# Performance work log

Hardware: AMD Instinct MI355X
Metric: run time of the kernel (lower is better)

Reference implementation:

```python
import jax, jax.numpy as jnp
import numpy as np

B, D, N, H, K = 4, 1024, 4096, 16, 128
DH = D // H  # per-head dim (note: torch view splits D as (DH, H) in that order)
BN_EPS = 1e-3


def conv1(x, w, b):
    # 1x1 Conv1d == channel matmul: x [B,Cin,N], w [Cout,Cin], b [Cout]
    return jnp.einsum('oi,bin->bon', w, x) + b[None, :, None]


def setup_inputs() -> dict:
    key = jax.random.key(0)
    ks = jax.random.split(key, 16)
    s = 0.02
    proj_std = 1.0 / np.sqrt(K)  # init_() uniform(-1/sqrt(k), 1/sqrt(k))
    return {
        'x': jax.random.normal(ks[0], (B, D, N), jnp.float32),
        'source': jax.random.normal(ks[1], (B, D, N), jnp.float32),
        'to_q_w': jax.random.normal(ks[2], (D, D), jnp.float32) * s,
        'to_q_b': jnp.zeros((D,), jnp.float32),
        'to_k_w': jax.random.normal(ks[3], (D, D), jnp.float32) * s,
        'to_k_b': jnp.zeros((D,), jnp.float32),
        'proj_k': jax.random.uniform(ks[4], (N, K), jnp.float32, -proj_std, proj_std),
        'merge_w': jax.random.normal(ks[5], (D, D), jnp.float32) * s,
        'merge_b': jnp.zeros((D,), jnp.float32),
        'mlp_w1': jax.random.normal(ks[6], (2 * D, 2 * D), jnp.float32) * s,
        'mlp_b1': jnp.zeros((2 * D,), jnp.float32),
        'bn_gamma': jnp.ones((2 * D,), jnp.float32),
        'bn_beta': jnp.zeros((2 * D,), jnp.float32),
        'bn_mean': jnp.zeros((2 * D,), jnp.float32),
        'bn_var': jnp.ones((2 * D,), jnp.float32),
        'mlp_w2': jax.random.normal(ks[7], (D, 2 * D), jnp.float32) * s,
        'mlp_b2': jnp.zeros((D,), jnp.float32),
    }


def reference(x, source, to_q_w, to_q_b, to_k_w, to_k_b, proj_k, merge_w, merge_b,
              mlp_w1, mlp_b1, bn_gamma, bn_beta, bn_mean, bn_var, mlp_w2, mlp_b2):
    b = x.shape[0]
    q = conv1(x, to_q_w, to_q_b)          # [B,D,N]
    k = conv1(source, to_k_w, to_k_b)     # [B,D,M]
    v = k                                  # share_kv=True
    # Linformer sequence-length reduction: M -> K (proj_v == proj_k when shared)
    k = jnp.einsum('bdm,mk->bdk', k, proj_k)   # [B,D,K]
    v = jnp.einsum('bdm,mk->bdk', v, proj_k)   # [B,D,K]
    # torch .view(B, dim, heads, -1): channel axis split as (DH, H)
    qh = q.reshape(b, DH, H, N)
    kh = k.reshape(b, DH, H, K)
    vh = v.reshape(b, DH, H, K)
    scores = jnp.einsum('bdhn,bdhk->bhnk', qh, kh) / (DH ** 0.5)
    prob = jax.nn.softmax(scores, axis=-1)      # [B,H,N,K], small K
    msg = jnp.einsum('bhnk,bdhk->bdhn', prob, vh).reshape(b, D, N)
    msg = conv1(msg, merge_w, merge_b)
    # MLP([2D, 2D, D]): conv -> BN(eval, eps=1e-3) -> ReLU -> conv
    h = jnp.concatenate([x, msg], axis=1)       # [B,2D,N]
    h = conv1(h, mlp_w1, mlp_b1)
    h = bn_gamma[None, :, None] * (h - bn_mean[None, :, None]) \
        * jax.lax.rsqrt(bn_var + BN_EPS)[None, :, None] + bn_beta[None, :, None]
    h = jax.nn.relu(h)
    return conv1(h, mlp_w2, mlp_b2)             # [B,D,N]
```

## Files before the change

### kernel.cpp

```cpp
#include <hip/hip_runtime.h>
#include <stdint.h>

typedef __bf16 bf16x8 __attribute__((ext_vector_type(8)));
typedef float f32x4 __attribute__((ext_vector_type(4)));

__device__ __forceinline__ unsigned short f2bf(float f) {
    union { float f; uint32_t i; } v;
    v.f = f;
    uint32_t x = v.i;
    return (unsigned short)((x + 0x7FFFu + ((x >> 16) & 1u)) >> 16);
}

typedef __attribute__((address_space(3))) unsigned int lds_u32;
typedef __attribute__((address_space(1))) const unsigned int glob_u32;
__device__ __forceinline__ void gld16(const unsigned short* g, unsigned short* l) {
    __builtin_amdgcn_global_load_lds((glob_u32*)g, (lds_u32*)l, 16, 0, 0);
}

__global__ __launch_bounds__(256) void prep_weights(
    const float* __restrict__ Wq, const float* __restrict__ Wk,
    const float* __restrict__ Wm, const float* __restrict__ W1,
    const float* __restrict__ W2, const float* __restrict__ bq,
    const float* __restrict__ bk,
    unsigned short* __restrict__ wqb, unsigned short* __restrict__ wkb,
    unsigned short* __restrict__ wmb, unsigned short* __restrict__ w1b,
    unsigned short* __restrict__ w2b, float* __restrict__ bqp,
    float* __restrict__ bkp)
{
    const int b = blockIdx.x, t = threadIdx.x;
    if (b < 2048) {
        const float* in = (b < 1024) ? Wq : Wk;
        unsigned short* out = (b < 1024) ? wqb : wkb;
        const int i = ((b & 1023) * 256 + t) * 4;
        const int row = i >> 10, col = i & 1023;
        const float4 v = *(const float4*)(in + ((row & 63) * 16 + (row >> 6)) * 1024 + col);
        out[i + 0] = f2bf(v.x); out[i + 1] = f2bf(v.y);
        out[i + 2] = f2bf(v.z); out[i + 3] = f2bf(v.w);
    } else if (b < 3072) {
        const int i = ((b - 2048) * 256 + t) * 4;
        const int row = i >> 10, c0 = i & 1023;
        const float* r = Wm + (size_t)row * 1024;
#pragma unroll
        for (int j = 0; j < 4; ++j) {
            const int c = c0 + j;
            wmb[i + j] = f2bf(r[(c & 63) * 16 + (c >> 6)]);
        }
    } else if (b < 7168) {
        const int i = ((b - 3072) * 256 + t) * 4;
        const float4 v = *(const float4*)(W1 + i);
        w1b[i + 0] = f2bf(v.x); w1b[i + 1] = f2bf(v.y);
        w1b[i + 2] = f2bf(v.z); w1b[i + 3] = f2bf(v.w);
    } else if (b < 9216) {
        const int i = ((b - 7168) * 256 + t) * 4;
        const float4 v = *(const float4*)(W2 + i);
        w2b[i + 0] = f2bf(v.x); w2b[i + 1] = f2bf(v.y);
        w2b[i + 2] = f2bf(v.z); w2b[i + 3] = f2bf(v.w);
    } else {
        const int o = (b - 9216) * 256 + t;
        const int src = (o & 63) * 16 + (o >> 6);
        bqp[o] = bq[src];
        bkp[o] = bk[src];
    }
}

__global__ __launch_bounds__(256) void cvt_transpose(
    const float* __restrict__ in, unsigned short* __restrict__ out,
    int R, int C)
{
    __shared__ unsigned short tile[32][33];
    const size_t bo = (size_t)blockIdx.z * R * C;
    const int c0 = blockIdx.x * 32, r0 = blockIdx.y * 32;
    const int tx = threadIdx.x & 31, ty = threadIdx.x >> 5;
#pragma unroll
    for (int i = 0; i < 4; ++i)
        tile[ty + i * 8][tx] = f2bf(in[bo + (size_t)(r0 + ty + i * 8) * C + (c0 + tx)]);
    __syncthreads();
#pragma unroll
    for (int i = 0; i < 4; ++i)
        out[bo + (size_t)(c0 + ty + i * 8) * R + (r0 + tx)] = tile[tx][ty + i * 8];
}

__global__ __launch_bounds__(256) void cvt_transpose_xs(
    const float* __restrict__ x, const float* __restrict__ s,
    unsigned short* __restrict__ xt, unsigned short* __restrict__ st)
{
    __shared__ unsigned short tile[32][33];
    const int z = blockIdx.z;
    const float* in = (z < 4) ? x : s;
    unsigned short* out = (z < 4) ? xt : st;
    const size_t bo = (size_t)(z & 3) * 1024 * 4096;
    const int c0 = blockIdx.x * 32, r0 = blockIdx.y * 32;
    const int tx = threadIdx.x & 31, ty = threadIdx.x >> 5;
#pragma unroll
    for (int i = 0; i < 4; ++i)
        tile[ty + i * 8][tx] = f2bf(in[bo + (size_t)(r0 + ty + i * 8) * 4096 + (c0 + tx)]);
    __syncthreads();
#pragma unroll
    for (int i = 0; i < 4; ++i)
        out[bo + (size_t)(c0 + ty + i * 8) * 1024 + (r0 + tx)] = tile[tx][ty + i * 8];
}

template<int LDA, int LDB, int LDC, int KD, int SPLIT, bool CONCAT>
__global__ __launch_bounds__(256) void gemm_bt(
    const unsigned short* __restrict__ A,
    const unsigned short* __restrict__ A2, int K1,
    const unsigned short* __restrict__ BT,
    unsigned short* __restrict__ C, float* __restrict__ Cf,
    long long strideA, long long strideB, long long strideC,
    const float* __restrict__ bias_m,
    const float* __restrict__ bias_n,
    const float* __restrict__ bn_g,
    const float* __restrict__ bn_b,
    const float* __restrict__ bn_mu,
    const float* __restrict__ bn_var)
{
    constexpr int KPB = KD / SPLIT;
    __shared__ __align__(16) unsigned short As[128 * 64];
    __shared__ __align__(16) unsigned short Bs[128 * 64];

    const int z = blockIdx.z;
    const int batch = z / SPLIT;
    const int kbase = (z % SPLIT) * KPB;
    const int m0 = blockIdx.y * 128, n0 = blockIdx.x * 128;
    const unsigned short* Ab  = A + (size_t)batch * strideA;
    const unsigned short* A2b = CONCAT ? A2 + (size_t)batch * strideA
                                       : (const unsigned short*)0;
    const unsigned short* Bb = BT + (size_t)batch * strideB;

    const int t = threadIdx.x;
    const int lane = t & 63, wid = t >> 6;
    const int wm = wid >> 1, wn = wid & 1;
    const int r16 = lane & 15, quad = lane >> 4;

    f32x4 acc[4][4];
    const f32x4 zf = {0.f, 0.f, 0.f, 0.f};
#pragma unroll
    for (int i = 0; i < 4; ++i)
#pragma unroll
        for (int j = 0; j < 4; ++j) acc[i][j] = zf;

    for (int kt = kbase; kt < kbase + KPB; kt += 64) {
        const unsigned short* Asrc = Ab;
        int kk = kt;
        if (CONCAT && kt >= K1) { Asrc = A2b; kk = kt - K1; }
#pragma unroll
        for (int i = 0; i < 4; ++i) {
            const int p = i * 256 + t;
            const int row = p >> 3, slot = p & 7;
            const int kc = (slot ^ (row & 7)) * 8;
            gld16(&Asrc[(size_t)(m0 + row) * LDA + kk + kc], &As[p * 8]);
            gld16(&Bb[(size_t)(n0 + row) * LDB + kt + kc], &Bs[p * 8]);
        }
        __syncthreads();
#pragma unroll
        for (int s = 0; s < 2; ++s) {
            bf16x8 af[4], bfb[4];
#pragma unroll
            for (int i = 0; i < 4; ++i) {
                const int ra = wm * 64 + i * 16 + r16;
                const int rb = wn * 64 + i * 16 + r16;
                af[i]  = *(const bf16x8*)&As[(ra * 8 + ((s * 4 + quad) ^ (ra & 7))) * 8];
                bfb[i] = *(const bf16x8*)&Bs[(rb * 8 + ((s * 4 + quad) ^ (rb & 7))) * 8];
            }
#pragma unroll
            for (int mi = 0; mi < 4; ++mi)
#pragma unroll
                for (int ni = 0; ni < 4; ++ni)
                    acc[mi][ni] = __builtin_amdgcn_mfma_f32_16x16x32_bf16(
                        af[mi], bfb[ni], acc[mi][ni], 0, 0, 0);
        }
        __syncthreads();
    }

    unsigned short* Cb = C ? C + (size_t)z * strideC : (unsigned short*)0;
    float* Cfb = Cf ? Cf + (size_t)z * strideC : (float*)0;
    const bool has_bn = (bn_g != 0);
#pragma unroll
    for (int ni = 0; ni < 4; ++ni) {
        const int gn = n0 + wn * 64 + ni * 16 + r16;
        const float addn = bias_n ? bias_n[gn] : 0.f;
        float g = 1.f, bb = 0.f, mu = 0.f, rstd = 1.f;
        if (has_bn) {
            g = bn_g[gn]; bb = bn_b[gn]; mu = bn_mu[gn];
            rstd = rsqrtf(bn_var[gn] + 1e-3f);
        }
#pragma unroll
        for (int mi = 0; mi < 4; ++mi) {
            const int gm0 = m0 + wm * 64 + mi * 16 + quad * 4;
#pragma unroll
            for (int r = 0; r < 4; ++r) {
                float v = acc[mi][ni][r] + addn;
                if (bias_m) v += bias_m[gm0 + r];
                if (has_bn) { v = g * (v - mu) * rstd + bb; v = fmaxf(v, 0.f); }
                const size_t idx = (size_t)(gm0 + r) * LDC + gn;
                if (Cfb) Cfb[idx] = v;
                else     Cb[idx]  = f2bf(v);
            }
        }
    }
}

__global__ __launch_bounds__(256) void reduce_kp(
    const float* __restrict__ acc, unsigned short* __restrict__ kpb)
{
    const int j = (blockIdx.x * 256 + threadIdx.x) * 4;
    const int b = j >> 17, jj = j & 131071;
    const float* base = acc + (size_t)b * 8 * 131072 + jj;
    float4 s = *(const float4*)base;
#pragma unroll
    for (int p = 1; p < 8; ++p) {
        const float4 v = *(const float4*)(base + (size_t)p * 131072);
        s.x += v.x; s.y += v.y; s.z += v.z; s.w += v.w;
    }
    kpb[j + 0] = f2bf(s.x); kpb[j + 1] = f2bf(s.y);
    kpb[j + 2] = f2bf(s.z); kpb[j + 3] = f2bf(s.w);
}

__global__ __launch_bounds__(256) void attn_fused(
    const unsigned short* __restrict__ qT,
    const unsigned short* __restrict__ kp,
    unsigned short* __restrict__ msgT)
{
    constexpr int QS = 72, KS = 72, VS = 136, PS = 136;
    __shared__ __align__(16) unsigned short QKP[128 * QS + 128 * KS];
    __shared__ __align__(16) unsigned short Vs[64 * VS];
    unsigned short* Qs = QKP;
    unsigned short* Ks = QKP + 128 * QS;
    unsigned short* Ps = QKP;

    const int t = threadIdx.x;
    const int lane = t & 63, w = t >> 6;
    const int r16 = lane & 15, quad = lane >> 4;
    const int h = blockIdx.y, n0 = blockIdx.x * 128;
    const size_t b = blockIdx.z;

    const unsigned short* qbase = qT + (b * 4096 + n0) * 1024 + h * 64;
    const unsigned short* kbase = kp + (b * 1024 + h * 64) * 128;

#pragma unroll
    for (int i = 0; i < 4; ++i) {
        const int c = i * 256 + t;
        const int n = c >> 3, dh0 = (c & 7) * 8;
        *(int4*)&Qs[n * QS + dh0] = *(const int4*)&qbase[(size_t)n * 1024 + dh0];
    }
#pragma unroll
    for (int i = 0; i < 4; ++i) {
        const int c = i * 256 + t;
        const int kkq = c & 3, dh = (c >> 2) & 63, kkh = c >> 8;
        const int kk0 = kkh * 32 + kkq * 8;
        const bf16x8 v = *(const bf16x8*)&kbase[(size_t)dh * 128 + kk0];
        *(bf16x8*)&Vs[dh * VS + kk0] = v;
        const unsigned short* vs = (const unsigned short*)&v;
#pragma unroll
        for (int j = 0; j < 8; ++j) Ks[(kk0 + j) * KS + dh] = vs[j];
    }
    __syncthreads();

    f32x4 S[2][8];
    const f32x4 zf = {0.f, 0.f, 0.f, 0.f};
#pragma unroll
    for (int mi = 0; mi < 2; ++mi)
#pragma unroll
        for (int ni = 0; ni < 8; ++ni) S[mi][ni] = zf;

    bf16x8 aq[2][2];
#pragma unroll
    for (int mi = 0; mi < 2; ++mi)
#pragma unroll
        for (int ks = 0; ks < 2; ++ks)
            aq[mi][ks] = *(const bf16x8*)&Qs[(w * 32 + mi * 16 + r16) * QS + ks * 32 + quad * 8];
#pragma unroll
    for (int ni = 0; ni < 8; ++ni) {
        const bf16x8 b0 = *(const bf16x8*)&Ks[(ni * 16 + r16) * KS + quad * 8];
        const bf16x8 b1 = *(const bf16x8*)&Ks[(ni * 16 + r16) * KS + 32 + quad * 8];
#pragma unroll
        for (int mi = 0; mi < 2; ++mi) {
            S[mi][ni] = __builtin_amdgcn_mfma_f32_16x16x32_bf16(aq[mi][0], b0, S[mi][ni], 0, 0, 0);
            S[mi][ni] = __builtin_amdgcn_mfma_f32_16x16x32_bf16(aq[mi][1], b1, S[mi][ni], 0, 0, 0);
        }
    }

    __syncthreads();

    float linv[2][4];
#pragma unroll
    for (int mi = 0; mi < 2; ++mi) {
        float e[8][4];
        float rs0 = 0.f, rs1 = 0.f, rs2 = 0.f, rs3 = 0.f;
#pragma unroll
        for (int ni = 0; ni < 8; ++ni) {
            e[ni][0] = __expf(S[mi][ni][0] * 0.125f); rs0 += e[ni][0];
            e[ni][1] = __expf(S[mi][ni][1] * 0.125f); rs1 += e[ni][1];
            e[ni][2] = __expf(S[mi][ni][2] * 0.125f); rs2 += e[ni][2];
            e[ni][3] = __expf(S[mi][ni][3] * 0.125f); rs3 += e[ni][3];
        }
        float rs[4] = {rs0, rs1, rs2, rs3};
#pragma unroll
        for (int r = 0; r < 4; ++r) {
            float s = rs[r];
            s += __shfl_xor(s, 1); s += __shfl_xor(s, 2);
            s += __shfl_xor(s, 4); s += __shfl_xor(s, 8);
            linv[mi][r] = 1.f / s;
        }
#pragma unroll
        for (int ni = 0; ni < 8; ++ni)
#pragma unroll
            for (int r = 0; r < 4; ++r)
                Ps[(w * 32 + mi * 16 + quad * 4 + r) * PS + ni * 16 + r16] = f2bf(e[ni][r]);
    }
    __syncthreads();

    f32x4 O[2][4];
#pragma unroll
    for (int mi = 0; mi < 2; ++mi)
#pragma unroll
        for (int ni = 0; ni < 4; ++ni) O[mi][ni] = zf;

    bf16x8 ap[2][4];
#pragma unroll
    for (int mi = 0; mi < 2; ++mi)
#pragma unroll
        for (int ks = 0; ks < 4; ++ks)
            ap[mi][ks] = *(const bf16x8*)&Ps[(w * 32 + mi * 16 + r16) * PS + ks * 32 + quad * 8];
#pragma unroll
    for (int ni = 0; ni < 4; ++ni)
#pragma unroll
        for (int ks = 0; ks < 4; ++ks) {
            const bf16x8 bv = *(const bf16x8*)&Vs[(ni * 16 + r16) * VS + ks * 32 + quad * 8];
#pragma unroll
            for (int mi = 0; mi < 2; ++mi)
                O[mi][ni] = __builtin_amdgcn_mfma_f32_16x16x32_bf16(ap[mi][ks], bv, O[mi][ni], 0, 0, 0);
        }

    unsigned short* ob = msgT + (b * 4096 + n0) * 1024 + h * 64;
#pragma unroll
    for (int mi = 0; mi < 2; ++mi)
#pragma unroll
        for (int ni = 0; ni < 4; ++ni)
#pragma unroll
            for (int r = 0; r < 4; ++r)
                ob[(size_t)(w * 32 + mi * 16 + quad * 4 + r) * 1024 + ni * 16 + r16] =
                    f2bf(O[mi][ni][r] * linv[mi][r]);
}

extern "C" void kernel_launch(void* const* d_in, const int* in_sizes, int n_in,
                              void* d_out, int out_size, void* d_ws, size_t ws_size,
                              hipStream_t stream)
{
    (void)in_sizes; (void)n_in; (void)out_size; (void)ws_size;
    const float* x    = (const float*)d_in[0];
    const float* srcp = (const float*)d_in[1];
    const float* Wq   = (const float*)d_in[2];
    const float* bq   = (const float*)d_in[3];
    const float* Wk   = (const float*)d_in[4];
    const float* bk   = (const float*)d_in[5];
    const float* proj = (const float*)d_in[6];
    const float* Wm   = (const float*)d_in[7];
    const float* bm   = (const float*)d_in[8];
    const float* W1   = (const float*)d_in[9];
    const float* b1   = (const float*)d_in[10];
    const float* gam  = (const float*)d_in[11];
    const float* bet  = (const float*)d_in[12];
    const float* mu   = (const float*)d_in[13];
    const float* var  = (const float*)d_in[14];
    const float* W2   = (const float*)d_in[15];
    const float* b2   = (const float*)d_in[16];
    float* out = (float*)d_out;
    unsigned short* ws = (unsigned short*)d_ws;

    const long long E = 16777216LL;
    unsigned short* xt  = ws;
    unsigned short* st  = xt + E;
    unsigned short* qt  = st + E;
    unsigned short* kc  = qt + E;
    unsigned short* ht  = kc + E;
    unsigned short* pT  = ht + 2 * E;
    unsigned short* kpb = pT + 524288;
    unsigned short* wqb = kpb + 524288;
    unsigned short* wkb = wqb + 1048576;
    unsigned short* wmb = wkb + 1048576;
    unsigned short* w1b = wmb + 1048576;
    unsigned short* w2b = w1b + 4194304;
    float* bqp = (float*)(w2b + 2097152);
    float* bkp = bqp + 1024;
    float* kpacc = (float*)ht;

    cvt_transpose_xs<<<dim3(128, 32, 8), 256, 0, stream>>>(x, srcp, xt, st);
    cvt_transpose<<<dim3(4, 128, 1), 256, 0, stream>>>(proj, pT, 4096, 128);
    prep_weights<<<9220, 256, 0, stream>>>(Wq, Wk, Wm, W1, W2, bq, bk,
                                           wqb, wkb, wmb, w1b, w2b, bqp, bkp);

    gemm_bt<1024, 1024, 1024, 1024, 1, false><<<dim3(8, 32, 4), 256, 0, stream>>>(
        xt, nullptr, 1024, wqb, qt, nullptr,
        4096LL * 1024, 0LL, 4096LL * 1024, nullptr, bqp,
        nullptr, nullptr, nullptr, nullptr);
    gemm_bt<1024, 1024, 4096, 1024, 1, false><<<dim3(32, 8, 4), 256, 0, stream>>>(
        wkb, nullptr, 1024, st, kc, nullptr,
        0LL, 4096LL * 1024, 1024LL * 4096, bkp, nullptr,
        nullptr, nullptr, nullptr, nullptr);
    gemm_bt<4096, 4096, 128, 4096, 8, false><<<dim3(1, 8, 32), 256, 0, stream>>>(
        kc, nullptr, 4096, pT, nullptr, kpacc,
        1024LL * 4096, 0LL, 1024LL * 128, nullptr, nullptr,
        nullptr, nullptr, nullptr, nullptr);
    reduce_kp<<<512, 256, 0, stream>>>(kpacc, kpb);
    attn_fused<<<dim3(32, 16, 4), 256, 0, stream>>>(qt, kpb, qt);
    gemm_bt<1024, 1024, 1024, 1024, 1, false><<<dim3(8, 32, 4), 256, 0, stream>>>(
        qt, nullptr, 1024, wmb, st, nullptr,
        4096LL * 1024, 0LL, 4096LL * 1024, nullptr, bm,
        nullptr, nullptr, nullptr, nullptr);
    gemm_bt<1024, 2048, 2048, 2048, 1, true><<<dim3(16, 32, 4), 256, 0, stream>>>(
        xt, st, 1024, w1b, ht, nullptr,
        4096LL * 1024, 0LL, 4096LL * 2048, nullptr, b1,
        gam, bet, mu, var);
    gemm_bt<2048, 2048, 4096, 2048, 1, false><<<dim3(32, 8, 4), 256, 0, stream>>>(
        w2b, nullptr, 2048, ht, nullptr, out,
        0LL, 4096LL * 2048, 1024LL * 4096, b2, nullptr,
        nullptr, nullptr, nullptr, nullptr);
}
```

Before: 727.0 us.

## Add 256x256 double-buffered 8-wave GEMM kernel for projection and MLP GEMMs

Introduces a new gemm256 kernel with 256x256 output tiles, 512 threads, double-buffered LDS filled by direct global-to-LDS loads, XOR-swizzled layout, interleaved load/MFMA phases with setprio, and an XCD-aware block remap. It replaces the previous gemm_bt launches for the Q, K, merge, and both MLP GEMMs. The aim is higher arithmetic intensity and better overlap of memory loads with MFMA work. It also uses much more LDS (128KB per block), which may limit occupancy, and the grids are smaller, which could leave CUs underused.

After: 667.8 us. -8.1%, faster.

```diff
diff --git a/kernel.cpp b/kernel.cpp
--- a/kernel.cpp
+++ b/kernel.cpp
@@ -199,6 +199,183 @@
         }
     }
 }
+
+#define BAR   __builtin_amdgcn_s_barrier()
+#define LGKM0 asm volatile("s_waitcnt lgkmcnt(0)" ::: "memory")
+#define PRIO1 __builtin_amdgcn_s_setprio(1)
+#define PRIO0 __builtin_amdgcn_s_setprio(0)
+
+#define ST_A(dst, kt, i0, i1) do {                                          \
+    const unsigned short* S_ = Ab; long long kk_ = (kt);                    \
+    if (CONCAT && (kt) >= K1) { S_ = A2b; kk_ = (kt) - K1; }                \
+    gld16(&S_[offA[i0] + kk_], (dst) + po[i0]);                             \
+    gld16(&S_[offA[i1] + kk_], (dst) + po[i1]); } while (0)
+
+#define ST_B(dst, kt, i0, i1) do {                                          \
+    gld16(&Bb[offB[i0] + (kt)], (dst) + po[i0]);                            \
+    gld16(&Bb[offB[i1] + (kt)], (dst) + po[i1]); } while (0)
+
+#define RD_A(mh, AC) do {                                                   \
+    _Pragma("unroll") for (int mi = 0; mi < 4; ++mi) {                      \
+        const int ra = wm * 128 + (mh) * 64 + mi * 16 + r16;                \
+        _Pragma("unroll") for (int ks = 0; ks < 2; ++ks) {                  \
+            const int c_ = ks * 4 + quad;                                   \
+            a[mi][ks] = *(const bf16x8*)&(AC)[(ra * 8 + (c_ ^ (ra & 7))) * 8]; \
+        } } } while (0)
+
+#define RD_B(np, BC) do {                                                   \
+    _Pragma("unroll") for (int i = 0; i < 2; ++i) {                         \
+        const int rb = wn * 64 + ((np) * 2 + i) * 16 + r16;                 \
+        _Pragma("unroll") for (int ks = 0; ks < 2; ++ks) {                  \
+            const int c_ = ks * 4 + quad;                                   \
+            b[(np) * 2 + i][ks] = *(const bf16x8*)&(BC)[(rb * 8 + (c_ ^ (rb & 7))) * 8]; \
+        } } } while (0)
+
+#define MFMA_PH(mh, np) do {                                                \
+    _Pragma("unroll") for (int mi = 0; mi < 4; ++mi)                        \
+    _Pragma("unroll") for (int i = 0; i < 2; ++i)                           \
+    _Pragma("unroll") for (int ks = 0; ks < 2; ++ks)                        \
+        acc[(mh) * 4 + mi][(np) * 2 + i] =                                  \
+            __builtin_amdgcn_mfma_f32_16x16x32_bf16(                        \
+                a[mi][ks], b[(np) * 2 + i][ks],                             \
+                acc[(mh) * 4 + mi][(np) * 2 + i], 0, 0, 0); } while (0)
+
+#define TILE_BODY(XV, AC, BC, AN, BN_) do {                                 \
+    const int kt1_ = ((XV) + 1) * 64, kt2_ = ((XV) + 2) * 64;               \
+    const bool g1_ = ((XV) + 1) < nt, g2_ = ((XV) + 2) < nt;                \
+         \
+    RD_A(0, AC); RD_B(0, BC);                                               \
+    if (g1_) ST_A(AN, kt1_, 1, 3);                                          \
+    BAR; LGKM0; PRIO1; MFMA_PH(0, 0); PRIO0; BAR;                           \
+       \
+    RD_B(1, BC);                                                            \
+    if (g2_) ST_A(AC, kt2_, 0, 2);                                          \
+    BAR; LGKM0; PRIO1; MFMA_PH(0, 1); PRIO0; BAR;                           \
+       \
+    RD_A(1, AC);                                                            \
+    if (g2_) ST_B(BC, kt2_, 0, 1);                                          \
+    BAR; LGKM0; PRIO1; MFMA_PH(1, 1); PRIO0; BAR;                           \
+           \
+    if (g2_) { ST_B(BC, kt2_, 2, 3);                                        \
+               asm volatile("s_waitcnt vmcnt(6)" ::: "memory"); }           \
+    else     { asm volatile("s_waitcnt vmcnt(0)" ::: "memory"); }           \
+    BAR; LGKM0; PRIO1; MFMA_PH(1, 0); PRIO0; BAR;                           \
+} while (0)
+
+template<int LDA, int LDB, int LDC, int KD, bool CONCAT>
+__global__ __launch_bounds__(512, 2) void gemm256(
+    const unsigned short* __restrict__ A,
+    const unsigned short* __restrict__ A2, int K1,
+    const unsigned short* __restrict__ BT,
+    unsigned short* __restrict__ C, float* __restrict__ Cf,
+    long long strideA, long long strideB, long long strideC,
+    const float* __restrict__ bias_m,
+    const float* __restrict__ bias_n,
+    const float* __restrict__ bn_g,
+    const float* __restrict__ bn_b,
+    const float* __restrict__ bn_mu,
+    const float* __restrict__ bn_var)
+{
+    static_assert(KD % 128 == 0, "nt must be even");
+    constexpr int nt = KD / 64;
+    constexpr int TILE = 256 * 64;
+    __shared__ __align__(16) unsigned short As[2 * TILE];
+    __shared__ __align__(16) unsigned short Bs[2 * TILE];
+    unsigned short* As0 = As;        unsigned short* As1 = As + TILE;
+    unsigned short* Bs0 = Bs;        unsigned short* Bs1 = Bs + TILE;
+
+    const int batch = blockIdx.z;
+    const int gx = gridDim.x;
+    const int nwg = gx * gridDim.y;
+    int flat = blockIdx.y * gx + blockIdx.x;
+    flat = (flat & 7) * (nwg >> 3) + (flat >> 3);
+    const int n0 = (flat % gx) * 256;
+    const int m0 = (flat / gx) * 256;
+
+    const unsigned short* Ab  = A + (size_t)batch * strideA;
+    const unsigned short* A2b = CONCAT ? A2 + (size_t)batch * strideA
+                                       : (const unsigned short*)0;
+    const unsigned short* Bb  = BT + (size_t)batch * strideB;
+
+    const int t = threadIdx.x;
+    const int lane = t & 63, wid = t >> 6;
+    const int wm = wid >> 2, wn = wid & 3;
+    const int r16 = lane & 15, quad = lane >> 4;
+
+    long long offA[4], offB[4];
+    int po[4];
+#pragma unroll
+    for (int i = 0; i < 4; ++i) {
+        const int p = i * 512 + t, row = p >> 3;
+        const int kc = ((p & 7) ^ (row & 7)) * 8;
+        po[i] = p * 8;
+        offA[i] = (long long)(m0 + row) * LDA + kc;
+        offB[i] = (long long)(n0 + row) * LDB + kc;
+    }
+
+    f32x4 acc[8][4];
+    const f32x4 zf = {0.f, 0.f, 0.f, 0.f};
+#pragma unroll
+    for (int i = 0; i < 8; ++i)
+#pragma unroll
+        for (int j = 0; j < 4; ++j) acc[i][j] = zf;
+
+    bf16x8 a[4][2], b[4][2];
+
+    ST_A(As0, 0, 0, 2);
+    ST_B(Bs0, 0, 0, 1);
+    ST_B(Bs0, 0, 2, 3);
+    ST_A(As0, 0, 1, 3);
+    ST_A(As1, 64, 0, 2);
+    ST_B(Bs1, 64, 0, 1);
+    ST_B(Bs1, 64, 2, 3);
+    asm volatile("s_waitcnt vmcnt(6)" ::: "memory");
+    BAR;
+
+#pragma unroll 1
+    for (int X2 = 0; X2 < nt; X2 += 2) {
+        TILE_BODY(X2,     As0, Bs0, As1, Bs1);
+        TILE_BODY(X2 + 1, As1, Bs1, As0, Bs0);
+    }
+
+    unsigned short* Cb = C ? C + (size_t)batch * strideC : (unsigned short*)0;
+    float* Cfb = Cf ? Cf + (size_t)batch * strideC : (float*)0;
+    const bool has_bn = (bn_g != 0);
+#pragma unroll
+    for (int ni = 0; ni < 4; ++ni) {
+        const int gn = n0 + wn * 64 + ni * 16 + r16;
+        const float addn = bias_n ? bias_n[gn] : 0.f;
+        float g = 1.f, bb = 0.f, mu = 0.f, rstd = 1.f;
+        if (has_bn) {
+            g = bn_g[gn]; bb = bn_b[gn]; mu = bn_mu[gn];
+            rstd = rsqrtf(bn_var[gn] + 1e-3f);
+        }
+#pragma unroll
+        for (int mi = 0; mi < 8; ++mi) {
+            const int gm0 = m0 + wm * 128 + mi * 16 + quad * 4;
+#pragma unroll
+            for (int r = 0; r < 4; ++r) {
+                float v = acc[mi][ni][r] + addn;
+                if (bias_m) v += bias_m[gm0 + r];
+                if (has_bn) { v = g * (v - mu) * rstd + bb; v = fmaxf(v, 0.f); }
+                const size_t idx = (size_t)(gm0 + r) * LDC + gn;
+                if (Cfb) Cfb[idx] = v;
+                else     Cb[idx]  = f2bf(v);
+            }
+        }
+    }
+}
+
+#undef TILE_BODY
+#undef MFMA_PH
+#undef RD_B
+#undef RD_A
+#undef ST_B
+#undef ST_A
+#undef PRIO0
+#undef PRIO1
+#undef LGKM0
+#undef BAR
 
 __global__ __launch_bounds__(256) void reduce_kp(
     const float* __restrict__ acc, unsigned short* __restrict__ kpb)
@@ -390,11 +567,11 @@
     prep_weights<<<9220, 256, 0, stream>>>(Wq, Wk, Wm, W1, W2, bq, bk,
                                            wqb, wkb, wmb, w1b, w2b, bqp, bkp);
 
-    gemm_bt<1024, 1024, 1024, 1024, 1, false><<<dim3(8, 32, 4), 256, 0, stream>>>(
+    gemm256<1024, 1024, 1024, 1024, false><<<dim3(4, 16, 4), 512, 0, stream>>>(
         xt, nullptr, 1024, wqb, qt, nullptr,
         4096LL * 1024, 0LL, 4096LL * 1024, nullptr, bqp,
         nullptr, nullptr, nullptr, nullptr);
-    gemm_bt<1024, 1024, 4096, 1024, 1, false><<<dim3(32, 8, 4), 256, 0, stream>>>(
+    gemm256<1024, 1024, 4096, 1024, false><<<dim3(16, 4, 4), 512, 0, stream>>>(
         wkb, nullptr, 1024, st, kc, nullptr,
         0LL, 4096LL * 1024, 1024LL * 4096, bkp, nullptr,
         nullptr, nullptr, nullptr, nullptr);
@@ -404,15 +581,15 @@
         nullptr, nullptr, nullptr, nullptr);
     reduce_kp<<<512, 256, 0, stream>>>(kpacc, kpb);
     attn_fused<<<dim3(32, 16, 4), 256, 0, stream>>>(qt, kpb, qt);
-    gemm_bt<1024, 1024, 1024, 1024, 1, false><<<dim3(8, 32, 4), 256, 0, stream>>>(
+    gemm256<1024, 1024, 1024, 1024, false><<<dim3(4, 16, 4), 512, 0, stream>>>(
         qt, nullptr, 1024, wmb, st, nullptr,
         4096LL * 1024, 0LL, 4096LL * 1024, nullptr, bm,
         nullptr, nullptr, nullptr, nullptr);
-    gemm_bt<1024, 2048, 2048, 2048, 1, true><<<dim3(16, 32, 4), 256, 0, stream>>>(
+    gemm256<1024, 2048, 2048, 2048, true><<<dim3(8, 16, 4), 512, 0, stream>>>(
         xt, st, 1024, w1b, ht, nullptr,
         4096LL * 1024, 0LL, 4096LL * 2048, nullptr, b1,
         gam, bet, mu, var);
-    gemm_bt<2048, 2048, 4096, 2048, 1, false><<<dim3(32, 8, 4), 256, 0, stream>>>(
+    gemm256<2048, 2048, 4096, 2048, false><<<dim3(16, 4, 4), 512, 0, stream>>>(
         w2b, nullptr, 2048, ht, nullptr, out,
         0LL, 4096LL * 2048, 1024LL * 4096, b2, nullptr,
         nullptr, nullptr, nullptr, nullptr);
```
